# Kernel tuning notes

Hardware: AMD Instinct MI355X
Metric: run time of the kernel (lower is better)

The kernel has to match this reference:

```python
import jax, jax.numpy as jnp
import numpy as np


def setup_inputs() -> dict:
    key = jax.random.key(0)
    ks = jax.random.split(key, 7)
    B, I, H, O, T = 1024, 2048, 2048, 2048, 30
    s = 1.0 / np.sqrt(H)
    return {
        "x": jax.random.normal(ks[0], (B, I), dtype=jnp.float32),
        "w_ih": jax.random.uniform(ks[1], (3 * H, I), jnp.float32, -s, s),
        "w_hh": jax.random.uniform(ks[2], (3 * H, H), jnp.float32, -s, s),
        "b_ih": jax.random.uniform(ks[3], (3 * H,), jnp.float32, -s, s),
        "b_hh": jax.random.uniform(ks[4], (3 * H,), jnp.float32, -s, s),
        "w_cls": jax.random.uniform(ks[5], (O, H), jnp.float32, -s, s),
        "b_cls": jax.random.uniform(ks[6], (O,), jnp.float32, -s, s),
        "num_timesteps": T,
    }


def reference(x, w_ih, w_hh, b_ih, b_hh, w_cls, b_cls, num_timesteps):
    # Original module never updates hidden_unit inside the loop, so every
    # timestep computes GRUCell(x, 0) -> identical output. Compute once,
    # broadcast across T (same math as the torch loop).
    # GRUCell with h=0: W_hh @ h vanishes; only bias_hh contributes.
    gi = x @ w_ih.T + b_ih                      # [B, 3H]
    i_r, i_z, i_n = jnp.split(gi, 3, axis=1)    # each [B, H]
    h_r, h_z, h_n = jnp.split(b_hh, 3)          # each [H]
    r = jax.nn.sigmoid(i_r + h_r)
    z = jax.nn.sigmoid(i_z + h_z)
    n = jnp.tanh(i_n + r * h_n)
    h_new = (1.0 - z) * n                       # + z * 0
    out = jax.nn.sigmoid(h_new @ w_cls.T + b_cls)  # [B, O]
    B, O = out.shape
    # torch stacks along dim 2 -> [B, O, T]; squeeze is a no-op for B,O,T > 1
    return jnp.broadcast_to(out[:, :, None], (B, O, num_timesteps))
```

## Files before the change

kernel.cpp:

```cpp
#include <hip/hip_runtime.h>
#include <hip/hip_bf16.h>
#include <math.h>

typedef __attribute__((ext_vector_type(8))) _Float16 f16x8;
typedef __attribute__((ext_vector_type(4))) float f32x4;

static __device__ __forceinline__ float sigmoidf_(float x) {
    return 1.0f / (1.0f + expf(-x));
}

#define GLL(src, dst) __builtin_amdgcn_global_load_lds(                         \
        (const __attribute__((address_space(1))) void*)(src),                   \
        (__attribute__((address_space(3))) void*)(dst), 16, 0, 0)

__global__ void cvt_all(const float* __restrict__ s0, _Float16* __restrict__ d0, int n0,
                        const float* __restrict__ s1, _Float16* __restrict__ d1, int n1,
                        const float* __restrict__ s2, _Float16* __restrict__ d2, int n2,
                        int ck01, int ck2)
{
    int c = blockIdx.x * 256 + threadIdx.x;
    const float* s; _Float16* d; int ck;
    if (c < n0)            { s = s0; d = d0; ck = ck01; }
    else if (c < n0 + n1)  { c -= n0; s = s1; d = d1; ck = ck01; }
    else                   { c -= n0 + n1; if (c >= n2) return; s = s2; d = d2; ck = ck2; }
    const int row = c / ck;
    const int kc  = c - row * ck;
    const int kcs = (kc & ~7) | ((kc & 7) ^ (row & 7));
    const float* sp = s + (size_t)c * 8;
    float4 v0 = *(const float4*)sp;
    float4 v1 = *(const float4*)(sp + 4);
    f16x8 h;
    h[0] = (_Float16)v0.x; h[1] = (_Float16)v0.y;
    h[2] = (_Float16)v0.z; h[3] = (_Float16)v0.w;
    h[4] = (_Float16)v1.x; h[5] = (_Float16)v1.y;
    h[6] = (_Float16)v1.z; h[7] = (_Float16)v1.w;
    *(f16x8*)(d + (size_t)row * ((size_t)ck * 8) + (size_t)kcs * 8) = h;
}

__launch_bounds__(256, 2)
__global__ void gemm1_gate(const _Float16* __restrict__ A,
                           const _Float16* __restrict__ W,
                           const float* __restrict__ b_ih,
                           const float* __restrict__ b_hh,
                           _Float16* __restrict__ hn,
                           int H, int I)
{
    constexpr int BM = 128, BNH = 32, BN = 96, BK = 64;
    constexpr int MR = 2, NR = 6;

    __shared__ _Float16 As[2][BM * BK];
    __shared__ _Float16 Bs[2][BN * BK];

    const int tid  = threadIdx.x;
    const int lane = tid & 63;
    const int wid  = tid >> 6;
    const int lr   = lane & 15;
    const int kb   = lane >> 4;
    const int brow = blockIdx.y * BM;
    const int h0   = blockIdx.x * BNH;

    const _Float16* asrc[4];
#pragma unroll
    for (int i = 0; i < 4; ++i) {
        const int c = i * 256 + tid;
        asrc[i] = A + (size_t)(brow + (c >> 3)) * I + (c & 7) * 8;
    }
    const _Float16* bsrc[3];
#pragma unroll
    for (int i = 0; i < 3; ++i) {
        const int c = i * 256 + tid;
        const int r = c >> 3, grp = r >> 5, hr = r & 31;
        bsrc[i] = W + (size_t)(grp * H + h0 + hr) * I + (c & 7) * 8;
    }

    f32x4 acc[MR][NR] = {};

    auto stage = [&](int buf, int kt) {
#pragma unroll
        for (int i = 0; i < 4; ++i)
            GLL(asrc[i] + (size_t)kt * BK, &As[buf][(i * 256 + tid) * 8]);
#pragma unroll
        for (int i = 0; i < 3; ++i)
            GLL(bsrc[i] + (size_t)kt * BK, &Bs[buf][(i * 256 + tid) * 8]);
    };
    auto compute = [&](int buf) {
#pragma unroll
        for (int ks = 0; ks < 2; ++ks) {
            f16x8 af[MR], bf[NR];
#pragma unroll
            for (int m = 0; m < MR; ++m) {
                const int row = wid * 32 + m * 16 + lr;
                af[m] = *(const f16x8*)&As[buf][row * BK + ((ks * 4 + kb) ^ (row & 7)) * 8];
            }
#pragma unroll
            for (int n = 0; n < NR; ++n) {
                const int row = n * 16 + lr;
                bf[n] = *(const f16x8*)&Bs[buf][row * BK + ((ks * 4 + kb) ^ (row & 7)) * 8];
            }
#pragma unroll
            for (int n = 0; n < NR; ++n)
#pragma unroll
                for (int m = 0; m < MR; ++m)
                    acc[m][n] = __builtin_amdgcn_mfma_f32_16x16x32_f16(af[m], bf[n], acc[m][n], 0, 0, 0);
        }
    };

    const int nt = I / BK;
    stage(0, 0);
    __syncthreads();
    int cur = 0;
    for (int t = 0; t < nt - 1; ++t) {
        stage(cur ^ 1, t + 1);
        compute(cur);
        __syncthreads();
        cur ^= 1;
    }
    compute(cur);

#pragma unroll
    for (int q = 0; q < 2; ++q) {
        const int h  = h0 + q * 16 + lr;
        const float br_ = b_ih[h]         + b_hh[h];
        const float bz_ = b_ih[H + h]     + b_hh[H + h];
        const float bn_ = b_ih[2 * H + h];
        const float hnb = b_hh[2 * H + h];
        const int hc  = h >> 3;
        const int hlo = h & 7;
#pragma unroll
        for (int m = 0; m < MR; ++m) {
            const int r0 = brow + wid * 32 + m * 16 + kb * 4;
#pragma unroll
            for (int j = 0; j < 4; ++j) {
                const int b = r0 + j;
                const float rr = sigmoidf_(acc[m][q][j]     + br_);
                const float zz = sigmoidf_(acc[m][q + 2][j] + bz_);
                const float hv = (1.0f - zz) * tanhf(acc[m][q + 4][j] + bn_ + rr * hnb);
                const int hcs = (hc & ~7) | ((hc & 7) ^ (b & 7));
                hn[(size_t)b * H + hcs * 8 + hlo] = (_Float16)hv;
            }
        }
    }
}

__launch_bounds__(256, 2)
__global__ void gemm2_bcast(const _Float16* __restrict__ A,
                            const _Float16* __restrict__ Bw,
                            const float* __restrict__ bias,
                            float* __restrict__ out,
                            int O, int K, int T)
{
    constexpr int BT = 64, BK = 64;
    constexpr int MR = 2, NR = 2;

    __shared__ _Float16 As[2][BT * BK];
    __shared__ _Float16 Bs[2][BT * BK];
    __shared__ float resS[64][65];

    const int tid  = threadIdx.x;
    const int lane = tid & 63;
    const int wid  = tid >> 6;
    const int wr   = wid >> 1;
    const int wc   = wid & 1;
    const int lr   = lane & 15;
    const int kb   = lane >> 4;
    const int brow = blockIdx.y * BT;
    const int bcol = blockIdx.x * BT;

    const _Float16* asrc[2];
    const _Float16* bsrc[2];
#pragma unroll
    for (int i = 0; i < 2; ++i) {
        const int c = i * 256 + tid;
        asrc[i] = A  + (size_t)(brow + (c >> 3)) * K + (c & 7) * 8;
        bsrc[i] = Bw + (size_t)(bcol + (c >> 3)) * K + (c & 7) * 8;
    }

    f32x4 acc[MR][NR] = {};

    auto stage = [&](int buf, int kt) {
#pragma unroll
        for (int i = 0; i < 2; ++i) {
            GLL(asrc[i] + (size_t)kt * BK, &As[buf][(i * 256 + tid) * 8]);
            GLL(bsrc[i] + (size_t)kt * BK, &Bs[buf][(i * 256 + tid) * 8]);
        }
    };
    auto compute = [&](int buf) {
#pragma unroll
        for (int ks = 0; ks < 2; ++ks) {
            f16x8 af[MR], bf[NR];
#pragma unroll
            for (int m = 0; m < MR; ++m) {
                const int row = wr * 32 + m * 16 + lr;
                af[m] = *(const f16x8*)&As[buf][row * BK + ((ks * 4 + kb) ^ (row & 7)) * 8];
            }
#pragma unroll
            for (int n = 0; n < NR; ++n) {
                const int row = wc * 32 + n * 16 + lr;
                bf[n] = *(const f16x8*)&Bs[buf][row * BK + ((ks * 4 + kb) ^ (row & 7)) * 8];
            }
#pragma unroll
            for (int n = 0; n < NR; ++n)
#pragma unroll
                for (int m = 0; m < MR; ++m)
                    acc[m][n] = __builtin_amdgcn_mfma_f32_16x16x32_f16(af[m], bf[n], acc[m][n], 0, 0, 0);
        }
    };

    const int nt = K / BK;
    stage(0, 0);
    __syncthreads();
    int cur = 0;
    for (int t = 0; t < nt - 1; ++t) {
        stage(cur ^ 1, t + 1);
        compute(cur);
        __syncthreads();
        cur ^= 1;
    }
    compute(cur);

#pragma unroll
    for (int m = 0; m < MR; ++m) {
        const int rl = wr * 32 + m * 16 + kb * 4;
#pragma unroll
        for (int n = 0; n < NR; ++n) {
            const int cl = wc * 32 + n * 16 + lr;
            const float bv = bias[bcol + cl];
#pragma unroll
            for (int j = 0; j < 4; ++j)
                resS[rl + j][cl] = sigmoidf_(acc[m][n][j] + bv);
        }
    }
    __syncthreads();

    if (!(T & 1)) {
        const int ppr = 32 * T;
        const int hT  = T >> 1;
        for (int j = tid; j < 64 * ppr; j += 256) {
            const int rl  = j / ppr;
            const int rem = j - rl * ppr;
            const int ol  = rem / hT;
            const float v = resS[rl][ol];
            float2* p = (float2*)out + ((size_t)(brow + rl) * O + bcol) * hT + rem;
            *p = make_float2(v, v);
        }
    } else {
        const int ppr = 64 * T;
        for (int j = tid; j < 64 * ppr; j += 256) {
            const int rl  = j / ppr;
            const int rem = j - rl * ppr;
            const int ol  = rem / T;
            out[((size_t)(brow + rl) * O + bcol) * T + rem] = resS[rl][ol];
        }
    }
}

extern "C" void kernel_launch(void* const* d_in, const int* in_sizes, int n_in,
                              void* d_out, int out_size, void* d_ws, size_t ws_size,
                              hipStream_t stream)
{
    const float* x     = (const float*)d_in[0];
    const float* w_ih  = (const float*)d_in[1];
    const float* b_ih  = (const float*)d_in[3];
    const float* b_hh  = (const float*)d_in[4];
    const float* w_cls = (const float*)d_in[5];
    const float* b_cls = (const float*)d_in[6];

    const int H3 = in_sizes[3];
    const int H  = H3 / 3;
    const int I  = in_sizes[1] / H3;
    const int B  = in_sizes[0] / I;
    const int O  = in_sizes[6];
    const int T  = out_size / (B * O);

    _Float16* x16    = (_Float16*)d_ws;
    _Float16* wcls16 = x16 + (size_t)B * I;
    _Float16* hn16   = wcls16 + (size_t)O * H;

    _Float16* wih16 = (_Float16*)d_out;

    dim3 blk(256);

    {
        const int n0 = B * I / 8, n1 = H3 * I / 8, n2 = O * H / 8;
        const int tot = n0 + n1 + n2;
        cvt_all<<<(tot + 255) / 256, blk, 0, stream>>>(x, x16, n0, w_ih, wih16, n1,
                                                       w_cls, wcls16, n2, I / 8, H / 8);
    }

    gemm1_gate<<<dim3(H / 32, B / 128), blk, 0, stream>>>(
        x16, wih16, b_ih, b_hh, hn16, H, I);

    gemm2_bcast<<<dim3(O / 64, B / 64), blk, 0, stream>>>(
        hn16, wcls16, b_cls, (float*)d_out, O, H, T);
}
```

Measured before the change: 416.0 us.

## Prefetch two stages ahead with explicit vmcnt waits and specialize T

Both GEMM kernels now keep two K-tiles in flight. Each loop waits on a partial vmcnt and uses raw s_barrier with sched_barrier instead of issuing one stage ahead under __syncthreads. The goal is to hide global-to-LDS load latency behind MFMA work. gemm2 also overlays the epilogue result buffer on the A/B staging LDS to shrink its shared memory footprint, and it is templated on T=30 so the broadcast-store index divisions become constant. The hand-written waitcnt counts depend on how many loads each stage issues, and they are fragile if the compiler or tile sizes change.

```diff
diff --git a/kernel.cpp b/kernel.cpp
--- a/kernel.cpp
+++ b/kernel.cpp
@@ -12,6 +12,11 @@
 #define GLL(src, dst) __builtin_amdgcn_global_load_lds(                         \
         (const __attribute__((address_space(1))) void*)(src),                   \
         (__attribute__((address_space(3))) void*)(dst), 16, 0, 0)
+
+#define WAITVM(N) do { asm volatile("s_waitcnt vmcnt(%0)" :: "i"(N) : "memory"); \
+                       __builtin_amdgcn_sched_barrier(0); } while (0)
+#define BARRIER() do { __builtin_amdgcn_s_barrier();                             \
+                       __builtin_amdgcn_sched_barrier(0); } while (0)
 
 __global__ void cvt_all(const float* __restrict__ s0, _Float16* __restrict__ d0, int n0,
                         const float* __restrict__ s1, _Float16* __restrict__ d1, int n1,
@@ -107,15 +112,17 @@
 
     const int nt = I / BK;
     stage(0, 0);
-    __syncthreads();
-    int cur = 0;
+    stage(1, 1);
     for (int t = 0; t < nt - 1; ++t) {
-        stage(cur ^ 1, t + 1);
-        compute(cur);
-        __syncthreads();
-        cur ^= 1;
-    }
-    compute(cur);
+        WAITVM(7);
+        BARRIER();
+        compute(t & 1);
+        BARRIER();
+        if (t + 2 < nt) stage(t & 1, t + 2);
+    }
+    WAITVM(0);
+    BARRIER();
+    compute((nt - 1) & 1);
 
 #pragma unroll
     for (int q = 0; q < 2; ++q) {
@@ -142,19 +149,21 @@
     }
 }
 
+template <int TT>
 __launch_bounds__(256, 2)
 __global__ void gemm2_bcast(const _Float16* __restrict__ A,
                             const _Float16* __restrict__ Bw,
                             const float* __restrict__ bias,
                             float* __restrict__ out,
-                            int O, int K, int T)
+                            int O, int K, int Tdyn)
 {
     constexpr int BT = 64, BK = 64;
     constexpr int MR = 2, NR = 2;
 
-    __shared__ _Float16 As[2][BT * BK];
-    __shared__ _Float16 Bs[2][BT * BK];
-    __shared__ float resS[64][65];
+    __shared__ __align__(16) char smem[2 * BT * BK * 2 * 2];
+    _Float16 (*As)[BT * BK] = (_Float16(*)[BT * BK])smem;
+    _Float16 (*Bs)[BT * BK] = (_Float16(*)[BT * BK])(smem + 2 * BT * BK * 2);
+    float (*resS)[65] = (float(*)[65])smem;
 
     const int tid  = threadIdx.x;
     const int lane = tid & 63;
@@ -208,15 +217,19 @@
 
     const int nt = K / BK;
     stage(0, 0);
+    stage(1, 1);
+    for (int t = 0; t < nt - 1; ++t) {
+        WAITVM(4);
+        BARRIER();
+        compute(t & 1);
+        BARRIER();
+        if (t + 2 < nt) stage(t & 1, t + 2);
+    }
+    WAITVM(0);
+    BARRIER();
+    compute((nt - 1) & 1);
+
     __syncthreads();
-    int cur = 0;
-    for (int t = 0; t < nt - 1; ++t) {
-        stage(cur ^ 1, t + 1);
-        compute(cur);
-        __syncthreads();
-        cur ^= 1;
-    }
-    compute(cur);
 
 #pragma unroll
     for (int m = 0; m < MR; ++m) {
@@ -232,9 +245,10 @@
     }
     __syncthreads();
 
+    const int T = (TT > 0) ? TT : Tdyn;
     if (!(T & 1)) {
+        const int hT  = T >> 1;
         const int ppr = 32 * T;
-        const int hT  = T >> 1;
         for (int j = tid; j < 64 * ppr; j += 256) {
             const int rl  = j / ppr;
             const int rem = j - rl * ppr;
@@ -290,6 +304,10 @@
     gemm1_gate<<<dim3(H / 32, B / 128), blk, 0, stream>>>(
         x16, wih16, b_ih, b_hh, hn16, H, I);
 
-    gemm2_bcast<<<dim3(O / 64, B / 64), blk, 0, stream>>>(
-        hn16, wcls16, b_cls, (float*)d_out, O, H, T);
-}
+    if (T == 30)
+        gemm2_bcast<30><<<dim3(O / 64, B / 64), blk, 0, stream>>>(
+            hn16, wcls16, b_cls, (float*)d_out, O, H, T);
+    else
+        gemm2_bcast<0><<<dim3(O / 64, B / 64), blk, 0, stream>>>(
+            hn16, wcls16, b_cls, (float*)d_out, O, H, T);
+}
```

Measured after the change: 391.9 us. 1.06x faster.
